# Kernel tuning notes

Hardware: AMD Instinct MI355X
Metric: run time of the kernel (lower is better)

## Reference

```python
import jax, jax.numpy as jnp
import numpy as np

D_MODEL = 1024
NUM_HEADS = 16
D_K = D_MODEL // NUM_HEADS
THETA = 10000.0


def _apply_rope(x, positions):
    # x: [B, H, S, d_k], positions: [B, S]
    dk = x.shape[-1]
    freq = 1.0 / (THETA ** (jnp.arange(0, dk, 2, dtype=jnp.float32) / dk))  # [dk/2]
    ang = positions.astype(jnp.float32)[:, None, :, None] * freq  # [B,1,S,dk/2]
    cos, sin = jnp.cos(ang), jnp.sin(ang)
    x_even = x[..., 0::2]
    x_odd = x[..., 1::2]
    re = x_even * cos - x_odd * sin
    ro = x_even * sin + x_odd * cos
    # interleave back: [..., dk/2, 2] -> [..., dk]
    return jnp.stack([re, ro], axis=-1).reshape(x.shape)


def setup_inputs() -> dict:
    key = jax.random.key(0)
    kx, kq, kk, kv, ko = jax.random.split(key, 5)
    B, S = 2, 2048
    std = (2.0 / (D_MODEL + D_MODEL)) ** 0.5
    x = jax.random.normal(kx, (B, S, D_MODEL), dtype=jnp.float32)
    Wq = jax.random.normal(kq, (D_MODEL, D_MODEL), dtype=jnp.float32) * std
    Wk = jax.random.normal(kk, (D_MODEL, D_MODEL), dtype=jnp.float32) * std
    Wv = jax.random.normal(kv, (D_MODEL, D_MODEL), dtype=jnp.float32) * std
    Wo = jax.random.normal(ko, (D_MODEL, D_MODEL), dtype=jnp.float32) * std
    token_positions = jnp.tile(jnp.arange(S, dtype=jnp.int32)[None, :], (B, 1))
    return {"x": x, "Wq": Wq, "Wk": Wk, "Wv": Wv, "Wo": Wo,
            "token_positions": token_positions}


def reference(x, Wq, Wk, Wv, Wo, token_positions):
    B, S, D = x.shape
    H, dk = NUM_HEADS, D_K
    scale = 1.0 / np.sqrt(dk)
    # Linear is y = x @ W.T with W:[d_out, d_in]
    q = jnp.einsum('bsd,ed->bse', x, Wq).reshape(B, S, H, dk).transpose(0, 2, 1, 3)
    k = jnp.einsum('bsd,ed->bse', x, Wk).reshape(B, S, H, dk).transpose(0, 2, 1, 3)
    v = jnp.einsum('bsd,ed->bse', x, Wv).reshape(B, S, H, dk).transpose(0, 2, 1, 3)
    q = _apply_rope(q, token_positions)
    k = _apply_rope(k, token_positions)
    scores = jnp.einsum('bhqd,bhkd->bhqk', q, k) * scale  # [B,H,S,S]
    causal = jnp.tril(jnp.ones((S, S), dtype=bool))
    scores = jnp.where(causal[None, None, :, :], scores, -jnp.inf)
    probs = jax.nn.softmax(scores, axis=-1)
    attn = jnp.einsum('bhqk,bhkd->bhqd', probs, v)  # [B,H,S,dk]
    attn = attn.transpose(0, 2, 1, 3).reshape(B, S, D)
    return jnp.einsum('bsd,ed->bse', attn, Wo)
```

## Files before the change

kernel.cpp:

```cpp
#include <hip/hip_runtime.h>
#include <hip/hip_bf16.h>
#include <math.h>

#define B_  2
#define S_  2048
#define H_  16
#define D_  1024
#define DK_ 64

typedef __attribute__((ext_vector_type(8))) short bf16x8;
typedef __attribute__((ext_vector_type(8))) unsigned short ushort8v;
typedef __attribute__((ext_vector_type(4))) float f32x4;

__device__ __forceinline__ unsigned short f2bf(float f) {
  unsigned u = __float_as_uint(f);
  unsigned r = (u + 0x7FFFu + ((u >> 16) & 1u)) >> 16;
  return (unsigned short)r;
}
__device__ __forceinline__ unsigned pack_trunc(float lo, float hi) {
  return (__float_as_uint(lo) >> 16) | (__float_as_uint(hi) & 0xffff0000u);
}
__device__ __forceinline__ float fast_exp2(float x) {
#if __has_builtin(__builtin_amdgcn_exp2f)
  return __builtin_amdgcn_exp2f(x);
#else
  return __expf(x * 0.69314718056f);
#endif
}
__device__ __forceinline__ void gload_lds16(const unsigned short* g,
                                            unsigned short* l) {
  __builtin_amdgcn_global_load_lds(
      (const __attribute__((address_space(1))) unsigned int*)(const void*)g,
      (__attribute__((address_space(3))) unsigned int*)(void*)l, 16, 0, 0);
}

__global__ __launch_bounds__(256)
void cast5_bf16(const float* __restrict__ x,  const float* __restrict__ wq,
                const float* __restrict__ wk, const float* __restrict__ wv,
                const float* __restrict__ wo,
                unsigned short* __restrict__ xb,  unsigned short* __restrict__ wqb,
                unsigned short* __restrict__ wkb, unsigned short* __restrict__ wvb,
                unsigned short* __restrict__ wob)
{
  const int idx = blockIdx.x;
  const float* s; unsigned short* d; int lblk;
  if (idx < 2048) { s = x; d = xb; lblk = idx; }
  else {
    int t = idx - 2048;
    int w = t >> 9;
    lblk  = t & 511;
    s = (w == 0) ? wq  : (w == 1) ? wk  : (w == 2) ? wv  : wo;
    d = (w == 0) ? wqb : (w == 1) ? wkb : (w == 2) ? wvb : wob;
  }
  size_t i0 = ((size_t)lblk * 256 + threadIdx.x) * 8;
  float4 v0 = *(const float4*)(s + i0);
  float4 v1 = *(const float4*)(s + i0 + 4);
  ushort8v o;
  o[0] = f2bf(v0.x); o[1] = f2bf(v0.y); o[2] = f2bf(v0.z); o[3] = f2bf(v0.w);
  o[4] = f2bf(v1.x); o[5] = f2bf(v1.y); o[6] = f2bf(v1.z); o[7] = f2bf(v1.w);
  *(ushort8v*)(d + i0) = o;
}

__global__ __launch_bounds__(256)
void gemm_qkv(const unsigned short* __restrict__ A,
              const unsigned short* __restrict__ W0,
              const unsigned short* __restrict__ W1,
              const unsigned short* __restrict__ W2,
              unsigned short* __restrict__ qh,
              unsigned short* __restrict__ kh,
              unsigned short* __restrict__ vt,
              const int* __restrict__ tp)
{
  const int z = blockIdx.z;
  const unsigned short* W = (z == 0) ? W0 : (z == 1) ? W1 : W2;

  __shared__ unsigned short As[128 * 32];
  __shared__ unsigned short Bs[128 * 32];

  const int tid   = threadIdx.x;
  const int wave  = tid >> 6;
  const int lane  = tid & 63;
  const int quad  = lane >> 4;
  const int col16 = lane & 15;
  const int row0  = blockIdx.y * 128;
  const int col0  = blockIdx.x * 128;
  const int wr    = (wave >> 1) * 64;
  const int wc    = (wave & 1) * 64;

  const int srow = wave * 16 + (lane >> 2);
  const int scol = ((lane & 3) ^ ((lane >> 2) & 3)) * 8;
  const unsigned short* gA = A + (size_t)(row0 + srow) * D_ + scol;
  const unsigned short* gB = W + (size_t)(col0 + srow) * D_ + scol;
  unsigned short* lA0 = &As[(wave * 16) * 32];
  unsigned short* lA1 = &As[(wave * 16 + 64) * 32];
  unsigned short* lB0 = &Bs[(wave * 16) * 32];
  unsigned short* lB1 = &Bs[(wave * 16 + 64) * 32];

  f32x4 acc[4][4];
  #pragma unroll
  for (int mt = 0; mt < 4; ++mt)
    #pragma unroll
    for (int nt = 0; nt < 4; ++nt)
      #pragma unroll
      for (int r = 0; r < 4; ++r) acc[mt][nt][r] = 0.f;

  const int jx = (quad ^ (col16 & 3)) * 8;

  for (int k0 = 0; k0 < D_; k0 += 32) {
    __syncthreads();
    gload_lds16(gA + k0,                   lA0);
    gload_lds16(gA + (size_t)64 * D_ + k0, lA1);
    gload_lds16(gB + k0,                   lB0);
    gload_lds16(gB + (size_t)64 * D_ + k0, lB1);
    __syncthreads();

    bf16x8 af[4], bfr[4];
    #pragma unroll
    for (int mt = 0; mt < 4; ++mt)
      af[mt] = *(const bf16x8*)&As[(wr + mt * 16 + col16) * 32 + jx];
    #pragma unroll
    for (int nt = 0; nt < 4; ++nt)
      bfr[nt] = *(const bf16x8*)&Bs[(wc + nt * 16 + col16) * 32 + jx];

    #pragma unroll
    for (int mt = 0; mt < 4; ++mt)
      #pragma unroll
      for (int nt = 0; nt < 4; ++nt)
        acc[mt][nt] = __builtin_amdgcn_mfma_f32_16x16x32_bf16(
            af[mt], bfr[nt], acc[mt][nt], 0, 0, 0);
  }

  if (z == 2) {
    #pragma unroll
    for (int mt = 0; mt < 4; ++mt) {
      int row = row0 + wr + mt * 16 + quad * 4;
      int bb  = row >> 11;
      int sl  = row & (S_ - 1);
      #pragma unroll
      for (int nt = 0; nt < 4; ++nt) {
        int col = col0 + wc + nt * 16 + col16;
        int h = col >> 6, d = col & 63;
        ushort4 o;
        o.x = f2bf(acc[mt][nt][0]); o.y = f2bf(acc[mt][nt][1]);
        o.z = f2bf(acc[mt][nt][2]); o.w = f2bf(acc[mt][nt][3]);
        *(ushort4*)(vt + ((size_t)((bb << 4) + h) * DK_ + d) * S_ + sl) = o;
      }
    }
  } else {
    unsigned short* C = z ? kh : qh;
    const float qs = z ? 1.0f : 0.1803368801111204f;
    const float sgn = (col16 & 1) ? 1.f : -1.f;
    float freqr[4];
    #pragma unroll
    for (int nt = 0; nt < 4; ++nt) {
      int i = ((wc + nt * 16 + col16) & 63) >> 1;
      freqr[nt] = exp2f(-0.4152410118f * (float)i);
    }
    #pragma unroll
    for (int mt = 0; mt < 4; ++mt)
      #pragma unroll
      for (int r = 0; r < 4; ++r) {
        int row = row0 + wr + mt * 16 + quad * 4 + r;
        float p = (float)tp[row];
        #pragma unroll
        for (int nt = 0; nt < 4; ++nt) {
          int col = col0 + wc + nt * 16 + col16;
          float ang = p * freqr[nt];
          float sn = __sinf(ang), cs = __cosf(ang);
          float val = acc[mt][nt][r];
          float oth = __shfl_xor(val, 1);
          C[(size_t)row * D_ + col] = f2bf((val * cs + oth * sgn * sn) * qs);
        }
      }
  }
}

__global__ __launch_bounds__(256)
void gemm_wo(const unsigned short* __restrict__ A,
             const unsigned short* __restrict__ W,
             float* __restrict__ C)
{
  __shared__ unsigned short As[64 * 32];
  __shared__ unsigned short Bs[128 * 32];

  const int tid   = threadIdx.x;
  const int wave  = tid >> 6;
  const int lane  = tid & 63;
  const int quad  = lane >> 4;
  const int col16 = lane & 15;
  const int row0  = blockIdx.y * 64;
  const int col0  = blockIdx.x * 128;
  const int wr    = (wave >> 1) * 32;
  const int wc    = (wave & 1) * 64;

  const int srow = wave * 16 + (lane >> 2);
  const int scol = ((lane & 3) ^ ((lane >> 2) & 3)) * 8;
  const unsigned short* gA = A + (size_t)(row0 + srow) * D_ + scol;
  const unsigned short* gB = W + (size_t)(col0 + srow) * D_ + scol;
  unsigned short* lA0 = &As[(wave * 16) * 32];
  unsigned short* lB0 = &Bs[(wave * 16) * 32];
  unsigned short* lB1 = &Bs[(wave * 16 + 64) * 32];

  f32x4 acc[2][4];
  #pragma unroll
  for (int mt = 0; mt < 2; ++mt)
    #pragma unroll
    for (int nt = 0; nt < 4; ++nt)
      #pragma unroll
      for (int r = 0; r < 4; ++r) acc[mt][nt][r] = 0.f;

  const int jx = (quad ^ (col16 & 3)) * 8;

  for (int k0 = 0; k0 < D_; k0 += 32) {
    __syncthreads();
    gload_lds16(gA + k0,                   lA0);
    gload_lds16(gB + k0,                   lB0);
    gload_lds16(gB + (size_t)64 * D_ + k0, lB1);
    __syncthreads();

    bf16x8 af[2], bfr[4];
    #pragma unroll
    for (int mt = 0; mt < 2; ++mt)
      af[mt] = *(const bf16x8*)&As[(wr + mt * 16 + col16) * 32 + jx];
    #pragma unroll
    for (int nt = 0; nt < 4; ++nt)
      bfr[nt] = *(const bf16x8*)&Bs[(wc + nt * 16 + col16) * 32 + jx];

    #pragma unroll
    for (int mt = 0; mt < 2; ++mt)
      #pragma unroll
      for (int nt = 0; nt < 4; ++nt)
        acc[mt][nt] = __builtin_amdgcn_mfma_f32_16x16x32_bf16(
            af[mt], bfr[nt], acc[mt][nt], 0, 0, 0);
  }

  #pragma unroll
  for (int mt = 0; mt < 2; ++mt)
    #pragma unroll
    for (int r = 0; r < 4; ++r) {
      int row = row0 + wr + mt * 16 + quad * 4 + r;
      #pragma unroll
      for (int nt = 0; nt < 4; ++nt) {
        int col = col0 + wc + nt * 16 + col16;
        C[(size_t)row * D_ + col] = acc[mt][nt][r];
      }
    }
}

__device__ __forceinline__ void attn_side(
    const unsigned short* __restrict__ Ks, const unsigned short* __restrict__ Vs,
    unsigned short (* __restrict__ Pl)[72],
    const bf16x8* qf, f32x4* Oacc, float& l_i,
    int quad, int col, int qlocal, bool diag)
{
  const int jx = quad ^ (col & 7);
  f32x4 st[4];
  #pragma unroll
  for (int nb = 0; nb < 4; ++nb) {
    const int s0 = (nb * 16 + col) * 8 + jx;
    bf16x8 ka0 = *(const bf16x8*)(Ks + s0 * 8);
    bf16x8 ka1 = *(const bf16x8*)(Ks + (s0 ^ 4) * 8);
    f32x4 a = {-24.f, -24.f, -24.f, -24.f};
    a = __builtin_amdgcn_mfma_f32_16x16x32_bf16(ka0, qf[0], a, 0, 0, 0);
    a = __builtin_amdgcn_mfma_f32_16x16x32_bf16(ka1, qf[1], a, 0, 0, 0);
    st[nb] = a;
  }

  if (diag) {
    #pragma unroll
    for (int nb = 0; nb < 4; ++nb)
      #pragma unroll
      for (int r = 0; r < 4; ++r)
        if (nb * 16 + quad * 4 + r > qlocal) st[nb][r] = -1e30f;
  }

  float rsum = 0.f;
  #pragma unroll
  for (int nb = 0; nb < 4; ++nb)
    #pragma unroll
    for (int r = 0; r < 4; ++r) {
      float pv = fast_exp2(st[nb][r]);
      st[nb][r] = pv;
      rsum += pv;
    }
  rsum += __shfl_xor(rsum, 16);
  rsum += __shfl_xor(rsum, 32);
  l_i += rsum;

  #pragma unroll
  for (int nb = 0; nb < 4; ++nb) {
    uint2 pk;
    pk.x = pack_trunc(st[nb][0], st[nb][1]);
    pk.y = pack_trunc(st[nb][2], st[nb][3]);
    *(uint2*)&Pl[col][nb * 16 + quad * 4] = pk;
  }

  bf16x8 pf0 = *(const bf16x8*)&Pl[col][quad * 8];
  bf16x8 pf1 = *(const bf16x8*)&Pl[col][32 + quad * 8];
  #pragma unroll
  for (int nb = 0; nb < 4; ++nb) {
    const int s0 = (nb * 16 + col) * 8 + jx;
    bf16x8 va0 = *(const bf16x8*)(Vs + s0 * 8);
    bf16x8 va1 = *(const bf16x8*)(Vs + (s0 ^ 4) * 8);
    Oacc[nb] = __builtin_amdgcn_mfma_f32_16x16x32_bf16(va0, pf0, Oacc[nb], 0, 0, 0);
    Oacc[nb] = __builtin_amdgcn_mfma_f32_16x16x32_bf16(va1, pf1, Oacc[nb], 0, 0, 0);
  }
}

__global__ __launch_bounds__(256)
void attn_mfma(const unsigned short* __restrict__ Q,
               const unsigned short* __restrict__ K,
               const unsigned short* __restrict__ Vt,
               unsigned short* __restrict__ O)
{
  const int qtA  = blockIdx.x;
  const int qtB  = 31 - qtA;
  const int bh   = blockIdx.y;
  const int b    = bh >> 4, h = bh & 15;
  const int tid  = threadIdx.x;
  const int wave = tid >> 6;
  const int lane = tid & 63;
  const int quad = lane >> 4;
  const int col  = lane & 15;
  const int qlocal = wave * 16 + col;

  __shared__ unsigned short Ks[512 * 8];
  __shared__ unsigned short Vs[512 * 8];
  __shared__ unsigned short PlA[4][16][72];
  __shared__ unsigned short PlB[4][16][72];

  const size_t qkbase = (size_t)b * S_ * D_ + (size_t)h * DK_;
  const size_t vtbase = (size_t)bh * DK_ * S_;

  const int qrowA = qtA * 64 + qlocal;
  const int qrowB = qtB * 64 + qlocal;
  bf16x8 qfA[2], qfB[2];
  qfA[0] = *(const bf16x8*)(Q + qkbase + (size_t)qrowA * D_ + quad * 8);
  qfA[1] = *(const bf16x8*)(Q + qkbase + (size_t)qrowA * D_ + 32 + quad * 8);
  qfB[0] = *(const bf16x8*)(Q + qkbase + (size_t)qrowB * D_ + quad * 8);
  qfB[1] = *(const bf16x8*)(Q + qkbase + (size_t)qrowB * D_ + 32 + quad * 8);

  const int sr = tid >> 3;
  const int sj = (tid & 7) ^ (sr & 7);
  const unsigned short* gK = K + qkbase + (size_t)sr * D_ + sj * 8;
  const unsigned short* gV = Vt + vtbase + (size_t)sr * S_ + sj * 8;
  unsigned short* ldsK[2] = { &Ks[(wave * 64) * 8], &Ks[(256 + wave * 64) * 8] };
  unsigned short* ldsV[2] = { &Vs[(wave * 64) * 8], &Vs[(256 + wave * 64) * 8] };

  f32x4 OaccA[4], OaccB[4];
  #pragma unroll
  for (int nb = 0; nb < 4; ++nb)
    #pragma unroll
    for (int r = 0; r < 4; ++r) { OaccA[nb][r] = 0.f; OaccB[nb][r] = 0.f; }
  float lA = 0.f, lB = 0.f;

  for (int kt = 0; kt <= qtB; ++kt) {
    __syncthreads();
    #pragma unroll
    for (int p = 0; p < 2; ++p) {
      gload_lds16(gK + (size_t)(kt * 64 + p * 32) * D_, ldsK[p]);
      gload_lds16(gV + (size_t)(p * 32) * S_ + kt * 64, ldsV[p]);
    }
    __syncthreads();

    attn_side(Ks, Vs, PlB[wave], qfB, OaccB, lB, quad, col, qlocal,
              kt == qtB);
    if (kt <= qtA)
      attn_side(Ks, Vs, PlA[wave], qfA, OaccA, lA, quad, col, qlocal,
                kt == qtA);
  }

  const float invA = 1.0f / lA;
  const float invB = 1.0f / lB;
  #pragma unroll
  for (int nb = 0; nb < 4; ++nb) {
    int d = nb * 16 + quad * 4;
    ushort4 oa, ob;
    oa.x = f2bf(OaccA[nb][0] * invA); oa.y = f2bf(OaccA[nb][1] * invA);
    oa.z = f2bf(OaccA[nb][2] * invA); oa.w = f2bf(OaccA[nb][3] * invA);
    ob.x = f2bf(OaccB[nb][0] * invB); ob.y = f2bf(OaccB[nb][1] * invB);
    ob.z = f2bf(OaccB[nb][2] * invB); ob.w = f2bf(OaccB[nb][3] * invB);
    *(ushort4*)(O + (size_t)b * S_ * D_ + (size_t)qrowA * D_ + h * DK_ + d) = oa;
    *(ushort4*)(O + (size_t)b * S_ * D_ + (size_t)qrowB * D_ + h * DK_ + d) = ob;
  }
}

extern "C" void kernel_launch(void* const* d_in, const int* in_sizes, int n_in,
                              void* d_out, int out_size, void* d_ws, size_t ws_size,
                              hipStream_t stream)
{
  const float* x  = (const float*)d_in[0];
  const float* Wq = (const float*)d_in[1];
  const float* Wk = (const float*)d_in[2];
  const float* Wv = (const float*)d_in[3];
  const float* Wo = (const float*)d_in[4];
  const int*   tp = (const int*)d_in[5];
  float* out = (float*)d_out;

  const size_t NTOK = (size_t)B_ * S_ * D_;
  const size_t NW   = (size_t)D_ * D_;
  unsigned short* qh  = (unsigned short*)d_ws;
  unsigned short* kh  = qh + NTOK;
  unsigned short* vt  = kh + NTOK;
  unsigned short* xb  = vt + NTOK;
  unsigned short* wqb = xb + NTOK;
  unsigned short* wkb = wqb + NW;
  unsigned short* wvb = wkb + NW;
  unsigned short* wob = wvb + NW;
  unsigned short* ab  = xb;

  cast5_bf16<<<dim3(4096), 256, 0, stream>>>(
      x, Wq, Wk, Wv, Wo, xb, wqb, wkb, wvb, wob);

  gemm_qkv<<<dim3(D_ / 128, (B_ * S_) / 128, 3), 256, 0, stream>>>(
      xb, wqb, wkb, wvb, qh, kh, vt, tp);

  attn_mfma<<<dim3(16, B_ * H_), 256, 0, stream>>>(qh, kh, vt, ab);

  gemm_wo<<<dim3(D_ / 128, (B_ * S_) / 64), 256, 0, stream>>>(ab, wob, out);
}
```

Baseline: 197.1 us.

## Transpose V projection GEMM, stage positions in LDS, load 128 keys per barrier

The V projection now runs as W_v·xᵀ, swapping the operand and row/col roles for z==2. The vt output is then written with consecutive sequence positions across lanes instead of strided ushort4 stores. Token positions for RoPE are staged once in shared memory. The attention kernel loads two 64-key tiles per barrier pair into doubled K/V LDS buffers, halving synchronisations. The cost is more LDS per block, which may lower occupancy, plus scalar 2-byte stores in the V epilogue.

```diff
diff --git a/kernel.cpp b/kernel.cpp
--- a/kernel.cpp
+++ b/kernel.cpp
@@ -62,7 +62,7 @@
 }
 
 __global__ __launch_bounds__(256)
-void gemm_qkv(const unsigned short* __restrict__ A,
+void gemm_qkv(const unsigned short* __restrict__ A0,
               const unsigned short* __restrict__ W0,
               const unsigned short* __restrict__ W1,
               const unsigned short* __restrict__ W2,
@@ -72,25 +72,30 @@
               const int* __restrict__ tp)
 {
   const int z = blockIdx.z;
-  const unsigned short* W = (z == 0) ? W0 : (z == 1) ? W1 : W2;
 
   __shared__ unsigned short As[128 * 32];
   __shared__ unsigned short Bs[128 * 32];
+  __shared__ int tps[128];
 
   const int tid   = threadIdx.x;
   const int wave  = tid >> 6;
   const int lane  = tid & 63;
   const int quad  = lane >> 4;
   const int col16 = lane & 15;
-  const int row0  = blockIdx.y * 128;
-  const int col0  = blockIdx.x * 128;
   const int wr    = (wave >> 1) * 64;
   const int wc    = (wave & 1) * 64;
 
+  const int row0 = (z == 2) ? blockIdx.x * 128 : blockIdx.y * 128;
+  const int col0 = (z == 2) ? blockIdx.y * 128 : blockIdx.x * 128;
+  const unsigned short* Aptr = (z == 0) ? A0 : (z == 1) ? A0 : W2;
+  const unsigned short* Bptr = (z == 0) ? W0 : (z == 1) ? W1 : A0;
+
+  if (z < 2 && tid < 128) tps[tid] = tp[row0 + tid];
+
   const int srow = wave * 16 + (lane >> 2);
   const int scol = ((lane & 3) ^ ((lane >> 2) & 3)) * 8;
-  const unsigned short* gA = A + (size_t)(row0 + srow) * D_ + scol;
-  const unsigned short* gB = W + (size_t)(col0 + srow) * D_ + scol;
+  const unsigned short* gA = Aptr + (size_t)(row0 + srow) * D_ + scol;
+  const unsigned short* gB = Bptr + (size_t)(col0 + srow) * D_ + scol;
   unsigned short* lA0 = &As[(wave * 16) * 32];
   unsigned short* lA1 = &As[(wave * 16 + 64) * 32];
   unsigned short* lB0 = &Bs[(wave * 16) * 32];
@@ -132,20 +137,19 @@
 
   if (z == 2) {
     #pragma unroll
-    for (int mt = 0; mt < 4; ++mt) {
-      int row = row0 + wr + mt * 16 + quad * 4;
-      int bb  = row >> 11;
-      int sl  = row & (S_ - 1);
-      #pragma unroll
-      for (int nt = 0; nt < 4; ++nt) {
-        int col = col0 + wc + nt * 16 + col16;
-        int h = col >> 6, d = col & 63;
-        ushort4 o;
-        o.x = f2bf(acc[mt][nt][0]); o.y = f2bf(acc[mt][nt][1]);
-        o.z = f2bf(acc[mt][nt][2]); o.w = f2bf(acc[mt][nt][3]);
-        *(ushort4*)(vt + ((size_t)((bb << 4) + h) * DK_ + d) * S_ + sl) = o;
+    for (int mt = 0; mt < 4; ++mt)
+      #pragma unroll
+      for (int r = 0; r < 4; ++r) {
+        int c = row0 + wr + mt * 16 + quad * 4 + r;
+        int h = c >> 6, d = c & 63;
+        #pragma unroll
+        for (int nt = 0; nt < 4; ++nt) {
+          int t  = col0 + wc + nt * 16 + col16;
+          int bb = t >> 11, sl = t & (S_ - 1);
+          vt[((size_t)((bb << 4) + h) * DK_ + d) * S_ + sl] =
+              f2bf(acc[mt][nt][r]);
+        }
       }
-    }
   } else {
     unsigned short* C = z ? kh : qh;
     const float qs = z ? 1.0f : 0.1803368801111204f;
@@ -160,8 +164,9 @@
     for (int mt = 0; mt < 4; ++mt)
       #pragma unroll
       for (int r = 0; r < 4; ++r) {
-        int row = row0 + wr + mt * 16 + quad * 4 + r;
-        float p = (float)tp[row];
+        int rl  = wr + mt * 16 + quad * 4 + r;
+        int row = row0 + rl;
+        float p = (float)tps[rl];
         #pragma unroll
         for (int nt = 0; nt < 4; ++nt) {
           int col = col0 + wc + nt * 16 + col16;
@@ -324,8 +329,8 @@
   const int col  = lane & 15;
   const int qlocal = wave * 16 + col;
 
-  __shared__ unsigned short Ks[512 * 8];
-  __shared__ unsigned short Vs[512 * 8];
+  __shared__ unsigned short Ks[1024 * 8];
+  __shared__ unsigned short Vs[1024 * 8];
   __shared__ unsigned short PlA[4][16][72];
   __shared__ unsigned short PlB[4][16][72];
 
@@ -344,8 +349,6 @@
   const int sj = (tid & 7) ^ (sr & 7);
   const unsigned short* gK = K + qkbase + (size_t)sr * D_ + sj * 8;
   const unsigned short* gV = Vt + vtbase + (size_t)sr * S_ + sj * 8;
-  unsigned short* ldsK[2] = { &Ks[(wave * 64) * 8], &Ks[(256 + wave * 64) * 8] };
-  unsigned short* ldsV[2] = { &Vs[(wave * 64) * 8], &Vs[(256 + wave * 64) * 8] };
 
   f32x4 OaccA[4], OaccB[4];
   #pragma unroll
@@ -354,20 +357,35 @@
     for (int r = 0; r < 4; ++r) { OaccA[nb][r] = 0.f; OaccB[nb][r] = 0.f; }
   float lA = 0.f, lB = 0.f;
 
-  for (int kt = 0; kt <= qtB; ++kt) {
-    __syncthreads();
-    #pragma unroll
-    for (int p = 0; p < 2; ++p) {
-      gload_lds16(gK + (size_t)(kt * 64 + p * 32) * D_, ldsK[p]);
-      gload_lds16(gV + (size_t)(p * 32) * S_ + kt * 64, ldsV[p]);
+  const int nK128 = (qtB + 2) >> 1;
+
+  for (int m = 0; m < nK128; ++m) {
+    __syncthreads();
+    #pragma unroll
+    for (int half = 0; half < 2; ++half) {
+      const int kbase = m * 128 + half * 64;
+      #pragma unroll
+      for (int p = 0; p < 2; ++p) {
+        gload_lds16(gK + (size_t)(kbase + p * 32) * D_,
+                    &Ks[(size_t)half * 4096 + (size_t)(p * 256 + wave * 64) * 8]);
+        gload_lds16(gV + (size_t)(p * 32) * S_ + kbase,
+                    &Vs[(size_t)half * 4096 + (size_t)(p * 256 + wave * 64) * 8]);
+      }
     }
     __syncthreads();
 
-    attn_side(Ks, Vs, PlB[wave], qfB, OaccB, lB, quad, col, qlocal,
-              kt == qtB);
-    if (kt <= qtA)
-      attn_side(Ks, Vs, PlA[wave], qfA, OaccA, lA, quad, col, qlocal,
-                kt == qtA);
+    #pragma unroll
+    for (int half = 0; half < 2; ++half) {
+      const int g = 2 * m + half;
+      const unsigned short* KsH = Ks + half * 4096;
+      const unsigned short* VsH = Vs + half * 4096;
+      if (g <= qtB)
+        attn_side(KsH, VsH, PlB[wave], qfB, OaccB, lB, quad, col, qlocal,
+                  g == qtB);
+      if (g <= qtA)
+        attn_side(KsH, VsH, PlA[wave], qfA, OaccA, lA, quad, col, qlocal,
+                  g == qtA);
+    }
   }
 
   const float invA = 1.0f / lA;
```

Result: faster. 192.4 us (-2.4%).
